# Kernel tuning notes

Hardware: AMD Instinct MI355X
Metric: run time of the kernel (lower is better)

The kernel has to match this reference:

```python
import jax, jax.numpy as jnp
import numpy as np

D_MODEL = 1024
N_HEADS = 16
D_HEAD = D_MODEL // N_HEADS
B, T = 4, 2048


def layernorm(x, g, b, eps=1e-5):
    mu = jnp.mean(x, axis=-1, keepdims=True)
    var = jnp.mean((x - mu) ** 2, axis=-1, keepdims=True)
    return (x - mu) * jax.lax.rsqrt(var + eps) * g + b


def setup_inputs() -> dict:
    key = jax.random.key(0)
    ks = jax.random.split(key, 12)
    s_in = 1.0 / np.sqrt(D_MODEL)
    s_ff = 1.0 / np.sqrt(4 * D_MODEL)
    return {
        "x": jax.random.normal(ks[0], (B, T, D_MODEL), jnp.float32),
        "Wq": jax.random.normal(ks[1], (N_HEADS, D_MODEL, D_HEAD), jnp.float32) * s_in,
        "Wk": jax.random.normal(ks[2], (N_HEADS, D_MODEL, D_HEAD), jnp.float32) * s_in,
        "Wv": jax.random.normal(ks[3], (N_HEADS, D_MODEL, D_HEAD), jnp.float32) * s_in,
        "Wproj": jax.random.normal(ks[4], (D_MODEL, D_MODEL), jnp.float32) * s_in,
        "bproj": jnp.zeros((D_MODEL,), jnp.float32),
        "W1": jax.random.normal(ks[5], (D_MODEL, 4 * D_MODEL), jnp.float32) * s_in,
        "b1": jnp.zeros((4 * D_MODEL,), jnp.float32),
        "W2": jax.random.normal(ks[6], (4 * D_MODEL, D_MODEL), jnp.float32) * s_ff,
        "b2": jnp.zeros((D_MODEL,), jnp.float32),
        "g1": jnp.ones((D_MODEL,), jnp.float32),
        "beta1": jnp.zeros((D_MODEL,), jnp.float32),
        "g2": jnp.ones((D_MODEL,), jnp.float32),
        "beta2": jnp.zeros((D_MODEL,), jnp.float32),
    }


def reference(x, Wq, Wk, Wv, Wproj, bproj, W1, b1, W2, b2, g1, beta1, g2, beta2):
    Bb, Tt, C = x.shape
    # x = ln1(x); residual uses the NORMALIZED x (quirk of original module)
    x1 = layernorm(x, g1, beta1)
    # all heads at once: [B,H,T,Dh]
    q = jnp.einsum("btd,hdk->bhtk", x1, Wq)
    k = jnp.einsum("btd,hdk->bhtk", x1, Wk)
    v = jnp.einsum("btd,hdk->bhtk", x1, Wv)
    # NOTE: original scales by 1/sqrt(C) with C = d_model, not d_head
    wei = jnp.einsum("bhtk,bhsk->bhts", q, k) / np.sqrt(C).astype(np.float32)
    causal = jnp.tril(jnp.ones((Tt, Tt), bool))
    wei = jnp.where(causal, wei, -jnp.inf)
    wei = jax.nn.softmax(wei, axis=-1)
    attn = jnp.einsum("bhts,bhsk->bhtk", wei, v)  # [B,H,T,Dh]
    attn = attn.transpose(0, 2, 1, 3).reshape(Bb, Tt, C)  # concat heads
    sa = attn @ Wproj + bproj
    x2 = x1 + sa
    # x = ln2(x); residual again uses the normalized tensor
    x3 = layernorm(x2, g2, beta2)
    h = jax.nn.relu(x3 @ W1 + b1)
    ff = h @ W2 + b2
    return x3 + ff
```

## Files before the change

kernel.cpp:

```cpp
#include <hip/hip_runtime.h>
#include <cstdint>

typedef _Float16 f16;
typedef __attribute__((ext_vector_type(8))) _Float16 f16x8;
typedef __attribute__((ext_vector_type(4))) _Float16 f16x4;
typedef __attribute__((ext_vector_type(2))) _Float16 f16x2;
typedef __attribute__((ext_vector_type(4))) float f32x4;
typedef __attribute__((ext_vector_type(16))) float f32x16;

#define D_MODEL 1024
#define T_SEQ   2048
#define NTOK    8192
#define DFF     4096
#define DHEAD   64

struct alignas(16) H8 { f16 h[8]; };

__device__ __forceinline__ void load_lds16(const void* gp, void* lp) {
  __builtin_amdgcn_global_load_lds(
      (const __attribute__((address_space(1))) unsigned int*)(unsigned long long)(uintptr_t)gp,
      (__attribute__((address_space(3))) unsigned int*)(unsigned int)(uintptr_t)lp,
      16, 0, 0);
}

__device__ __forceinline__ void phase_bar() {
  asm volatile("" ::: "memory");
  __builtin_amdgcn_sched_barrier(0);
  __builtin_amdgcn_s_barrier();
  __builtin_amdgcn_sched_barrier(0);
  asm volatile("" ::: "memory");
}

__device__ __forceinline__ void wait_vm2() {
  asm volatile("s_waitcnt vmcnt(2)" ::: "memory");
  __builtin_amdgcn_sched_barrier(0);
}
__device__ __forceinline__ void wait_vm0() {
  asm volatile("s_waitcnt vmcnt(0)" ::: "memory");
  __builtin_amdgcn_sched_barrier(0);
}

__global__ __launch_bounds__(256) void transpose_pack(
    const float* __restrict__ in, f16* __restrict__ out,
    int rows, int cols, long long in_slice, long long out_slice)
{
  __shared__ float tile[32][33];
  const float* inp = in + (size_t)blockIdx.z * in_slice;
  f16* outp = out + (size_t)blockIdx.z * out_slice;
  int r0 = blockIdx.x * 32, c0 = blockIdx.y * 32;
  int tx = threadIdx.x & 31, ty = threadIdx.x >> 5;
  #pragma unroll
  for (int i = 0; i < 4; ++i)
    tile[ty + i*8][tx] = inp[(size_t)(r0 + ty + i*8)*cols + c0 + tx];
  __syncthreads();
  #pragma unroll
  for (int i = 0; i < 4; ++i)
    outp[(size_t)(c0 + ty + i*8)*rows + r0 + tx] = (f16)tile[tx][ty + i*8];
}

__global__ __launch_bounds__(256) void ln_kernel(
    const float* __restrict__ x, const float* __restrict__ g, const float* __restrict__ b,
    float* __restrict__ outf, f16* __restrict__ outh)
{
  int row = blockIdx.x;
  const float* xr = x + (size_t)row * D_MODEL;
  int tid = threadIdx.x;
  float v[4];
  float s = 0.f;
  #pragma unroll
  for (int i = 0; i < 4; ++i) { v[i] = xr[tid + i*256]; s += v[i]; }
  #pragma unroll
  for (int off = 32; off > 0; off >>= 1) s += __shfl_down(s, off, 64);
  __shared__ float red1[4], red2[4];
  if ((tid & 63) == 0) red1[tid >> 6] = s;
  __syncthreads();
  float mean = (red1[0] + red1[1] + red1[2] + red1[3]) * (1.f / D_MODEL);
  float s2 = 0.f;
  #pragma unroll
  for (int i = 0; i < 4; ++i) { float d = v[i] - mean; s2 += d * d; }
  #pragma unroll
  for (int off = 32; off > 0; off >>= 1) s2 += __shfl_down(s2, off, 64);
  if ((tid & 63) == 0) red2[tid >> 6] = s2;
  __syncthreads();
  float var = (red2[0] + red2[1] + red2[2] + red2[3]) * (1.f / D_MODEL);
  float rstd = rsqrtf(var + 1e-5f);
  #pragma unroll
  for (int i = 0; i < 4; ++i) {
    int c = tid + i*256;
    float y = (v[i] - mean) * rstd * g[c] + b[c];
    outf[(size_t)row*D_MODEL + c] = y;
    outh[(size_t)row*D_MODEL + c] = (f16)y;
  }
}


#define STAGE_H(gbase, h, ldst, k0)                                            \
  { _Pragma("unroll")                                                          \
    for (int j_ = 0; j_ < 2; ++j_) {                                           \
      int c_  = tid + j_*512;                                                  \
      int rr_ = c_ >> 3;                                                       \
      int cg_ = (c_ & 7) ^ (rr_ & 7);                                          \
      load_lds16((gbase) + (size_t)((h)*128 + rr_) * K + (k0) + cg_*8,         \
                 (ldst) + (h)*128*64 + (size_t)(c_ & ~63) * 8);                \
    } }

#define LDS_A(bsel, mp)                                                        \
  { _Pragma("unroll")                                                          \
    for (int i_ = 0; i_ < 2; ++i_)                                             \
      _Pragma("unroll")                                                        \
      for (int ks_ = 0; ks_ < 4; ++ks_)                                        \
        fa[i_][ks_] = *(const f16x8*)(&As[bsel][                               \
            (wm + ((mp)*2 + i_)*32 + rl)*64 + (((ks_*2 + hl) ^ sw)*8)]); }

#define LDS_B(bsel, ni, fb)                                                    \
  { _Pragma("unroll")                                                          \
    for (int ks_ = 0; ks_ < 4; ++ks_)                                          \
      fb[ks_] = *(const f16x8*)(&Bs[bsel][                                     \
          (wn + (ni)*32 + rl)*64 + (((ks_*2 + hl) ^ sw)*8)]); }

#define MFMA8(mp, ni, fb)                                                      \
  { __builtin_amdgcn_s_setprio(1);                                             \
    _Pragma("unroll")                                                          \
    for (int ks_ = 0; ks_ < 4; ++ks_) {                                        \
      acc[(mp)*2+0][ni] = __builtin_amdgcn_mfma_f32_32x32x16_f16(              \
          fa[0][ks_], fb[ks_], acc[(mp)*2+0][ni], 0, 0, 0);                    \
      acc[(mp)*2+1][ni] = __builtin_amdgcn_mfma_f32_32x32x16_f16(              \
          fa[1][ks_], fb[ks_], acc[(mp)*2+1][ni], 0, 0, 0);                    \
    }                                                                          \
    __builtin_amdgcn_s_setprio(0); }

template<int MODE, int BN>
__global__ __launch_bounds__(512, 2) void gemm8(
    const f16* __restrict__ A, const f16* __restrict__ BT, int K,
    const float* __restrict__ bias, const float* __restrict__ resid,
    float* __restrict__ outf, f16* __restrict__ o0, f16* __restrict__ o1, f16* __restrict__ o2)
{
  constexpr int BM  = 256;
  constexpr int NWN = BN / 64;
  constexpr int MI  = (BM / (8 / NWN)) / 32;

  __shared__ __align__(16) f16 As[2][BM * 64];
  __shared__ __align__(16) f16 Bs[2][BN * 64];

  int tid  = threadIdx.x;
  int lane = tid & 63;
  int wave = tid >> 6;
  int rl = lane & 31, hl = lane >> 5;
  int sw = rl & 7;
  int wmi = wave / NWN, wni = wave % NWN;
  int wm = wmi * (MI * 32), wn = wni * 64;

  int gx  = gridDim.x;
  int nwg = gx * gridDim.y;
  int lin = blockIdx.x + gx * blockIdx.y;
  int sid = (nwg & 7) == 0 ? ((lin & 7) * (nwg >> 3) + (lin >> 3)) : lin;
  int bx  = sid % gx, by = sid / gx;

  size_t row0 = (size_t)bx * BM, col0 = (size_t)by * BN;
  const f16* a_base = A  + row0 * K;
  const f16* b_base = BT + col0 * K;
  int NT = K >> 6;

  f32x16 acc[MI][2];
  #pragma unroll
  for (int i = 0; i < MI; ++i)
    #pragma unroll
    for (int j = 0; j < 2; ++j)
      acc[i][j] = (f32x16)(0.f);

  f16x8 fa[2][4], fb0[4], fb1[4];

  if constexpr (BN == 256) {
    STAGE_H(a_base, 0, &As[0][0], 0);
    STAGE_H(a_base, 1, &As[0][0], 0);
    STAGE_H(b_base, 0, &Bs[0][0], 0);
    STAGE_H(b_base, 1, &Bs[0][0], 0);
    if (NT > 1) { STAGE_H(a_base, 0, &As[1][0], 64); wait_vm2(); }
    else        { wait_vm0(); }
    phase_bar();

    for (int t = 0; t < NT; ++t) {
      int cur = t & 1, nxt = cur ^ 1;
      int k1 = (t + 1) << 6, k2 = (t + 2) << 6;
      bool s1 = (t + 1) < NT, s2 = (t + 2) < NT;
      LDS_A(cur, 0); LDS_B(cur, 0, fb0);
      if (s1) STAGE_H(a_base, 1, &As[nxt][0], k1);
      phase_bar();
      MFMA8(0, 0, fb0);
      phase_bar();
      LDS_B(cur, 1, fb1);
      if (s1) STAGE_H(b_base, 0, &Bs[nxt][0], k1);
      phase_bar();
      MFMA8(0, 1, fb1);
      phase_bar();
      LDS_A(cur, 1);
      if (s1) STAGE_H(b_base, 1, &Bs[nxt][0], k1);
      phase_bar();
      MFMA8(1, 0, fb0);
      phase_bar();
      if (s2) STAGE_H(a_base, 0, &As[cur][0], k2);
      phase_bar();
      MFMA8(1, 1, fb1);
      if (s2) wait_vm2(); else wait_vm0();
      phase_bar();
    }
  } else {
    STAGE_H(a_base, 0, &As[0][0], 0);
    STAGE_H(a_base, 1, &As[0][0], 0);
    STAGE_H(b_base, 0, &Bs[0][0], 0);
    if (NT > 1) { STAGE_H(a_base, 0, &As[1][0], 64); wait_vm2(); }
    else        { wait_vm0(); }
    phase_bar();

    for (int t = 0; t < NT; t += 2) {
      int k1 = (t + 1) << 6, k2 = (t + 2) << 6, k3 = (t + 3) << 6;
      bool s1 = (t + 1) < NT, s2 = (t + 2) < NT, s3 = (t + 3) < NT;
      LDS_A(0, 0); LDS_B(0, 0, fb0);
      if (s1) { STAGE_H(a_base, 1, &As[1][0], k1); STAGE_H(b_base, 0, &Bs[1][0], k1); }
      phase_bar();
      MFMA8(0, 0, fb0);
      phase_bar();
      LDS_B(0, 1, fb1);
      if (s2) STAGE_H(a_base, 0, &As[0][0], k2);
      phase_bar();
      MFMA8(0, 1, fb1);
      if (s2) wait_vm2(); else wait_vm0();
      phase_bar();
      if (!s1) break;
      LDS_A(1, 0); LDS_B(1, 0, fb0);
      if (s2) { STAGE_H(a_base, 1, &As[0][0], k2); STAGE_H(b_base, 0, &Bs[0][0], k2); }
      phase_bar();
      MFMA8(0, 0, fb0);
      phase_bar();
      LDS_B(1, 1, fb1);
      if (s3) STAGE_H(a_base, 0, &As[1][0], k3);
      phase_bar();
      MFMA8(0, 1, fb1);
      if (s3) wait_vm2(); else wait_vm0();
      phase_bar();
    }
  }

  int rb = hl * 4;
  #pragma unroll
  for (int mi = 0; mi < MI; ++mi) {
    #pragma unroll
    for (int ni = 0; ni < 2; ++ni) {
      #pragma unroll
      for (int r = 0; r < 16; ++r) {
        size_t grow = row0 + wm + mi*32 + rb + (r & 3) + 8 * (r >> 2);
        size_t gcol = col0 + wn + ni*32 + rl;
        float v = acc[mi][ni][r];
        if constexpr (MODE == 0) {
          int sel = (int)(gcol >> 10);
          int hh  = ((int)gcol >> 6) & 15;
          int dd  = (int)gcol & 63;
          f16* dst = (sel == 0) ? o0 : ((sel == 1) ? o1 : o2);
          if (sel == 0) v *= 0.045084229f;
          size_t bh = (grow >> 11) * 16 + hh;
          dst[(bh * T_SEQ + (grow & 2047)) * DHEAD + dd] = (f16)v;
        } else if constexpr (MODE == 1 || MODE == 3) {
          size_t idx = grow * D_MODEL + gcol;
          outf[idx] = v + bias[gcol] + resid[idx];
        } else {
          float t = v + bias[gcol];
          o0[grow * (size_t)DFF + gcol] = (f16)(t > 0.f ? t : 0.f);
        }
      }
    }
  }
}

__global__ __launch_bounds__(256) void attn_mfma(
    const f16* __restrict__ qb, const f16* __restrict__ kb,
    const f16* __restrict__ vb, f16* __restrict__ attnb)
{
  constexpr int KT  = 64;
  constexpr int LDK = 72;
  __shared__ __align__(16) f16 Kl[KT * LDK];
  __shared__ __align__(16) f16 Vt[DHEAD * LDK];
  __shared__ __align__(16) f16 Pt[4 * 32 * LDK];

  int tid  = threadIdx.x;
  int lane = tid & 63, wave = tid >> 6;
  int n    = lane & 15, quad = lane >> 4;
  int quad4 = quad * 4;
  int bh   = blockIdx.y;

  const f16* qg = qb + (size_t)bh * T_SEQ * DHEAD;
  const f16* kg = kb + (size_t)bh * T_SEQ * DHEAD;
  const f16* vg = vb + (size_t)bh * T_SEQ * DHEAD;
  f16* Ptw = Pt + wave * 32 * LDK;
  size_t orow = (size_t)(bh >> 4) * T_SEQ;
  int hcol = (bh & 15) * DHEAD;

  #pragma unroll
  for (int pass = 0; pass < 2; ++pass) {
    int qi = pass == 0 ? (15 - (int)blockIdx.x) : (int)blockIdx.x;
    int qw = qi * 128 + wave * 32;

    f16x8 qfrag[2][2];
    #pragma unroll
    for (int ni = 0; ni < 2; ++ni)
      #pragma unroll
      for (int kj = 0; kj < 2; ++kj)
        qfrag[ni][kj] = *(const f16x8*)(qg + (size_t)(qw + ni*16 + n)*DHEAD + kj*32 + quad*8);

    f32x4 o[2][4];
    #pragma unroll
    for (int mb = 0; mb < 2; ++mb)
      #pragma unroll
      for (int di = 0; di < 4; ++di) o[mb][di] = f32x4{0.f,0.f,0.f,0.f};
    float lsum[2] = {0.f, 0.f};

    int ntiles = 2 * qi + 2;
    for (int kt = 0; kt < ntiles; ++kt) {
      int kt0 = kt * KT;
      __syncthreads();
      #pragma unroll
      for (int it = 0; it < 2; ++it) {
        int idx = tid + it * 256;
        int key = idx >> 3, dq = idx & 7;
        *(uint4*)(Kl + key * LDK + dq * 8) =
            *(const uint4*)(kg + (size_t)(kt0 + key) * DHEAD + dq * 8);
      }
      {
        int kp = tid & 31, dblk = tid >> 5;
        const f16* v0 = vg + (size_t)(kt0 + 2*kp) * DHEAD + dblk * 8;
        H8 va = *(const H8*)v0;
        H8 vbv = *(const H8*)(v0 + DHEAD);
        #pragma unroll
        for (int e = 0; e < 8; ++e) {
          f16x2 pk2; pk2[0] = va.h[e]; pk2[1] = vbv.h[e];
          *(f16x2*)(Vt + (dblk*8 + e) * LDK + 2*kp) = pk2;
        }
      }
      __syncthreads();

      if (kt0 > qw + 31) continue;
      bool need_mask = (kt0 + KT - 1) > qw;

      f32x4 st[4][2];
      #pragma unroll
      for (int mi = 0; mi < 4; ++mi)
        #pragma unroll
        for (int ni = 0; ni < 2; ++ni) st[mi][ni] = f32x4{0.f,0.f,0.f,0.f};
      #pragma unroll
      for (int kj = 0; kj < 2; ++kj) {
        #pragma unroll
        for (int mi = 0; mi < 4; ++mi) {
          f16x8 kf = *(const f16x8*)(Kl + (mi*16 + n) * LDK + kj*32 + quad*8);
          #pragma unroll
          for (int ni = 0; ni < 2; ++ni)
            st[mi][ni] = __builtin_amdgcn_mfma_f32_16x16x32_f16(kf, qfrag[ni][kj], st[mi][ni], 0, 0, 0);
        }
      }

      #pragma unroll
      for (int ni = 0; ni < 2; ++ni) {
        #pragma unroll
        for (int mi = 0; mi < 4; ++mi) {
          f16x4 pk;
          #pragma unroll
          for (int r = 0; r < 4; ++r) {
            float sv = st[mi][ni][r];
            if (need_mask) {
              int key = kt0 + mi*16 + quad4 + r;
              int qq  = qw  + ni*16 + n;
              if (key > qq) sv = -1e30f;
            }
            float p = __builtin_amdgcn_exp2f(sv);
            lsum[ni] += p;
            pk[r] = (f16)p;
          }
          *(f16x4*)(Ptw + (ni*16 + n) * LDK + mi*16 + quad4) = pk;
        }
      }

      #pragma unroll
      for (int kj = 0; kj < 2; ++kj) {
        f16x8 pf[2];
        #pragma unroll
        for (int mb = 0; mb < 2; ++mb)
          pf[mb] = *(const f16x8*)(Ptw + (mb*16 + n) * LDK + kj*32 + quad*8);
        #pragma unroll
        for (int di = 0; di < 4; ++di) {
          f16x8 vf = *(const f16x8*)(Vt + (di*16 + n) * LDK + kj*32 + quad*8);
          #pragma unroll
          for (int mb = 0; mb < 2; ++mb)
            o[mb][di] = __builtin_amdgcn_mfma_f32_16x16x32_f16(pf[mb], vf, o[mb][di], 0, 0, 0);
        }
      }
    }

    #pragma unroll
    for (int ni = 0; ni < 2; ++ni) {
      lsum[ni] += __shfl_xor(lsum[ni], 16, 64);
      lsum[ni] += __shfl_xor(lsum[ni], 32, 64);
    }
    #pragma unroll
    for (int mb = 0; mb < 2; ++mb) {
      #pragma unroll
      for (int r = 0; r < 4; ++r) {
        float lv  = __shfl(lsum[mb], quad4 + r, 64);
        float inv = 1.f / lv;
        int t = qw + mb*16 + quad4 + r;
        #pragma unroll
        for (int di = 0; di < 4; ++di)
          attnb[(orow + t) * D_MODEL + hcol + di*16 + n] = (f16)(o[mb][di][r] * inv);
      }
    }
  }
}

extern "C" void kernel_launch(void* const* d_in, const int* in_sizes, int n_in,
                              void* d_out, int out_size, void* d_ws, size_t ws_size,
                              hipStream_t stream)
{
  const float* x     = (const float*)d_in[0];
  const float* Wq    = (const float*)d_in[1];
  const float* Wk    = (const float*)d_in[2];
  const float* Wv    = (const float*)d_in[3];
  const float* Wproj = (const float*)d_in[4];
  const float* bproj = (const float*)d_in[5];
  const float* W1    = (const float*)d_in[6];
  const float* b1    = (const float*)d_in[7];
  const float* W2    = (const float*)d_in[8];
  const float* b2    = (const float*)d_in[9];
  const float* g1    = (const float*)d_in[10];
  const float* bt1   = (const float*)d_in[11];
  const float* g2    = (const float*)d_in[12];
  const float* bt2   = (const float*)d_in[13];
  float* out = (float*)d_out;
  (void)in_sizes; (void)n_in; (void)out_size; (void)ws_size;

  char* ws = (char*)d_ws;
  const size_t SZ_H16 = (size_t)NTOK * D_MODEL * 2;
  const size_t SZ_F32 = (size_t)NTOK * D_MODEL * 4;
  f16*   qb      = (f16*)(ws + 0);
  f16*   kb      = (f16*)(ws + 1 * SZ_H16);
  f16*   vb      = (f16*)(ws + 2 * SZ_H16);
  f16*   attnb   = (f16*)(ws + 3 * SZ_H16);
  f16*   hbuf    = (f16*)(ws + 0);
  float* x1f     = (float*)(ws + 4 * SZ_H16);
  f16*   x1h     = (f16*)(ws + 4 * SZ_H16 + SZ_F32);
  float* x3f     = (float*)(ws + 5 * SZ_H16 + SZ_F32);
  f16*   x3h     = (f16*)(ws + 5 * SZ_H16 + 2 * SZ_F32);
  char*  wb      = ws + 6 * SZ_H16 + 2 * SZ_F32;
  f16*   Wqkv_t  = (f16*)(wb);
  f16*   Wproj_t = (f16*)(wb + (size_t)3072*1024*2);
  f16*   W1_t    = (f16*)(wb + (size_t)(3072+1024)*1024*2);
  f16*   W2_t    = (f16*)(wb + (size_t)(3072+1024+4096)*1024*2);

  dim3 blk(256), blk5(512);
  transpose_pack<<<dim3(32, 2, 16), blk, 0, stream>>>(Wq, Wqkv_t,                 1024, 64,  65536, 65536);
  transpose_pack<<<dim3(32, 2, 16), blk, 0, stream>>>(Wk, Wqkv_t + 1024*1024,     1024, 64,  65536, 65536);
  transpose_pack<<<dim3(32, 2, 16), blk, 0, stream>>>(Wv, Wqkv_t + 2*1024*1024,   1024, 64,  65536, 65536);
  transpose_pack<<<dim3(32, 32, 1), blk, 0, stream>>>(Wproj, Wproj_t, 1024, 1024, 0, 0);
  transpose_pack<<<dim3(32, 128, 1), blk, 0, stream>>>(W1, W1_t, 1024, 4096, 0, 0);
  transpose_pack<<<dim3(128, 32, 1), blk, 0, stream>>>(W2, W2_t, 4096, 1024, 0, 0);
  ln_kernel<<<NTOK, blk, 0, stream>>>(x, g1, bt1, x1f, x1h);
  gemm8<0,128><<<dim3(32, 24), blk5, 0, stream>>>(x1h, Wqkv_t, 1024, nullptr, nullptr, nullptr, qb, kb, vb);
  attn_mfma<<<dim3(8, 64), blk, 0, stream>>>(qb, kb, vb, attnb);
  gemm8<1,128><<<dim3(32, 8), blk5, 0, stream>>>(attnb, Wproj_t, 1024, bproj, x1f, x1f, nullptr, nullptr, nullptr);
  ln_kernel<<<NTOK, blk, 0, stream>>>(x1f, g2, bt2, x3f, x3h);
  gemm8<2,256><<<dim3(32, 16), blk5, 0, stream>>>(x3h, W1_t, 1024, b1, nullptr, nullptr, hbuf, nullptr, nullptr);
  gemm8<3,128><<<dim3(32, 8), blk5, 0, stream>>>(hbuf, W2_t, 4096, b2, x3f, out, nullptr, nullptr, nullptr);
}
```

Measured before the change: 519.1 us.

## Split attention into one q-tile per block and prefetch next K/V tile

The attention kernel no longer processes two paired query tiles per block; instead the grid doubles to 16x64 blocks, each handling one query tile, with heaviest tiles scheduled first. K/V tiles for the next iteration are loaded into registers before the current tile's compute, hiding global-load latency behind MFMA work, and launch bounds request 4 blocks per CU. This trades the balanced-pair load scheme for more parallelism and software prefetch, at the cost of extra registers and potentially imbalanced block runtimes.

```diff
diff --git a/kernel.cpp b/kernel.cpp
--- a/kernel.cpp
+++ b/kernel.cpp
@@ -271,7 +271,7 @@
   }
 }
 
-__global__ __launch_bounds__(256) void attn_mfma(
+__global__ __launch_bounds__(256, 4) void attn_mfma(
     const f16* __restrict__ qb, const f16* __restrict__ kb,
     const f16* __restrict__ vb, f16* __restrict__ attnb)
 {
@@ -294,121 +294,129 @@
   size_t orow = (size_t)(bh >> 4) * T_SEQ;
   int hcol = (bh & 15) * DHEAD;
 
-  #pragma unroll
-  for (int pass = 0; pass < 2; ++pass) {
-    int qi = pass == 0 ? (15 - (int)blockIdx.x) : (int)blockIdx.x;
-    int qw = qi * 128 + wave * 32;
-
-    f16x8 qfrag[2][2];
-    #pragma unroll
-    for (int ni = 0; ni < 2; ++ni)
-      #pragma unroll
-      for (int kj = 0; kj < 2; ++kj)
-        qfrag[ni][kj] = *(const f16x8*)(qg + (size_t)(qw + ni*16 + n)*DHEAD + kj*32 + quad*8);
-
-    f32x4 o[2][4];
-    #pragma unroll
-    for (int mb = 0; mb < 2; ++mb)
-      #pragma unroll
-      for (int di = 0; di < 4; ++di) o[mb][di] = f32x4{0.f,0.f,0.f,0.f};
-    float lsum[2] = {0.f, 0.f};
-
-    int ntiles = 2 * qi + 2;
-    for (int kt = 0; kt < ntiles; ++kt) {
-      int kt0 = kt * KT;
-      __syncthreads();
-      #pragma unroll
-      for (int it = 0; it < 2; ++it) {
-        int idx = tid + it * 256;
-        int key = idx >> 3, dq = idx & 7;
-        *(uint4*)(Kl + key * LDK + dq * 8) =
-            *(const uint4*)(kg + (size_t)(kt0 + key) * DHEAD + dq * 8);
+  int qi = 15 - (int)blockIdx.x;
+  int qw = qi * 128 + wave * 32;
+
+  int skey0 = tid >> 3,  sdq = tid & 7;
+  int kp = tid & 31, dblk = tid >> 5;
+
+  f16x8 qfrag[2][2];
+  #pragma unroll
+  for (int ni = 0; ni < 2; ++ni)
+    #pragma unroll
+    for (int kj = 0; kj < 2; ++kj)
+      qfrag[ni][kj] = *(const f16x8*)(qg + (size_t)(qw + ni*16 + n)*DHEAD + kj*32 + quad*8);
+
+  f32x4 o[2][4];
+  #pragma unroll
+  for (int mb = 0; mb < 2; ++mb)
+    #pragma unroll
+    for (int di = 0; di < 4; ++di) o[mb][di] = f32x4{0.f,0.f,0.f,0.f};
+  float lsum[2] = {0.f, 0.f};
+
+  int ntiles = 2 * qi + 2;
+
+  uint4 kpre0, kpre1;
+  H8 vpa, vpb;
+  {
+    kpre0 = *(const uint4*)(kg + (size_t)skey0 * DHEAD + sdq * 8);
+    kpre1 = *(const uint4*)(kg + (size_t)(skey0 + 32) * DHEAD + sdq * 8);
+    const f16* v0 = vg + (size_t)(2*kp) * DHEAD + dblk * 8;
+    vpa = *(const H8*)v0;
+    vpb = *(const H8*)(v0 + DHEAD);
+  }
+
+  for (int kt = 0; kt < ntiles; ++kt) {
+    int kt0 = kt * KT;
+    __syncthreads();
+    *(uint4*)(Kl + skey0 * LDK + sdq * 8) = kpre0;
+    *(uint4*)(Kl + (skey0 + 32) * LDK + sdq * 8) = kpre1;
+    #pragma unroll
+    for (int e = 0; e < 8; ++e) {
+      f16x2 pk2; pk2[0] = vpa.h[e]; pk2[1] = vpb.h[e];
+      *(f16x2*)(Vt + (dblk*8 + e) * LDK + 2*kp) = pk2;
+    }
+    if (kt + 1 < ntiles) {
+      int nt0 = kt0 + KT;
+      kpre0 = *(const uint4*)(kg + (size_t)(nt0 + skey0) * DHEAD + sdq * 8);
+      kpre1 = *(const uint4*)(kg + (size_t)(nt0 + skey0 + 32) * DHEAD + sdq * 8);
+      const f16* v0 = vg + (size_t)(nt0 + 2*kp) * DHEAD + dblk * 8;
+      vpa = *(const H8*)v0;
+      vpb = *(const H8*)(v0 + DHEAD);
+    }
+    __syncthreads();
+
+    if (kt0 > qw + 31) continue;
+    bool need_mask = (kt0 + KT - 1) > qw;
+
+    f32x4 st[4][2];
+    #pragma unroll
+    for (int mi = 0; mi < 4; ++mi)
+      #pragma unroll
+      for (int ni = 0; ni < 2; ++ni) st[mi][ni] = f32x4{0.f,0.f,0.f,0.f};
+    #pragma unroll
+    for (int kj = 0; kj < 2; ++kj) {
+      #pragma unroll
+      for (int mi = 0; mi < 4; ++mi) {
+        f16x8 kf = *(const f16x8*)(Kl + (mi*16 + n) * LDK + kj*32 + quad*8);
+        #pragma unroll
+        for (int ni = 0; ni < 2; ++ni)
+          st[mi][ni] = __builtin_amdgcn_mfma_f32_16x16x32_f16(kf, qfrag[ni][kj], st[mi][ni], 0, 0, 0);
       }
-      {
-        int kp = tid & 31, dblk = tid >> 5;
-        const f16* v0 = vg + (size_t)(kt0 + 2*kp) * DHEAD + dblk * 8;
-        H8 va = *(const H8*)v0;
-        H8 vbv = *(const H8*)(v0 + DHEAD);
+    }
+
+    #pragma unroll
+    for (int ni = 0; ni < 2; ++ni) {
+      #pragma unroll
+      for (int mi = 0; mi < 4; ++mi) {
+        f16x4 pk;
         #pragma unroll
-        for (int e = 0; e < 8; ++e) {
-          f16x2 pk2; pk2[0] = va.h[e]; pk2[1] = vbv.h[e];
-          *(f16x2*)(Vt + (dblk*8 + e) * LDK + 2*kp) = pk2;
+        for (int r = 0; r < 4; ++r) {
+          float sv = st[mi][ni][r];
+          if (need_mask) {
+            int key = kt0 + mi*16 + quad4 + r;
+            int qq  = qw  + ni*16 + n;
+            if (key > qq) sv = -1e30f;
+          }
+          float p = __builtin_amdgcn_exp2f(sv);
+          lsum[ni] += p;
+          pk[r] = (f16)p;
         }
+        *(f16x4*)(Ptw + (ni*16 + n) * LDK + mi*16 + quad4) = pk;
       }
-      __syncthreads();
-
-      if (kt0 > qw + 31) continue;
-      bool need_mask = (kt0 + KT - 1) > qw;
-
-      f32x4 st[4][2];
-      #pragma unroll
-      for (int mi = 0; mi < 4; ++mi)
-        #pragma unroll
-        for (int ni = 0; ni < 2; ++ni) st[mi][ni] = f32x4{0.f,0.f,0.f,0.f};
-      #pragma unroll
-      for (int kj = 0; kj < 2; ++kj) {
-        #pragma unroll
-        for (int mi = 0; mi < 4; ++mi) {
-          f16x8 kf = *(const f16x8*)(Kl + (mi*16 + n) * LDK + kj*32 + quad*8);
-          #pragma unroll
-          for (int ni = 0; ni < 2; ++ni)
-            st[mi][ni] = __builtin_amdgcn_mfma_f32_16x16x32_f16(kf, qfrag[ni][kj], st[mi][ni], 0, 0, 0);
-        }
-      }
-
-      #pragma unroll
-      for (int ni = 0; ni < 2; ++ni) {
-        #pragma unroll
-        for (int mi = 0; mi < 4; ++mi) {
-          f16x4 pk;
-          #pragma unroll
-          for (int r = 0; r < 4; ++r) {
-            float sv = st[mi][ni][r];
-            if (need_mask) {
-              int key = kt0 + mi*16 + quad4 + r;
-              int qq  = qw  + ni*16 + n;
-              if (key > qq) sv = -1e30f;
-            }
-            float p = __builtin_amdgcn_exp2f(sv);
-            lsum[ni] += p;
-            pk[r] = (f16)p;
-          }
-          *(f16x4*)(Ptw + (ni*16 + n) * LDK + mi*16 + quad4) = pk;
-        }
-      }
-
-      #pragma unroll
-      for (int kj = 0; kj < 2; ++kj) {
-        f16x8 pf[2];
+    }
+
+    #pragma unroll
+    for (int kj = 0; kj < 2; ++kj) {
+      f16x8 pf[2];
+      #pragma unroll
+      for (int mb = 0; mb < 2; ++mb)
+        pf[mb] = *(const f16x8*)(Ptw + (mb*16 + n) * LDK + kj*32 + quad*8);
+      #pragma unroll
+      for (int di = 0; di < 4; ++di) {
+        f16x8 vf = *(const f16x8*)(Vt + (di*16 + n) * LDK + kj*32 + quad*8);
         #pragma unroll
         for (int mb = 0; mb < 2; ++mb)
-          pf[mb] = *(const f16x8*)(Ptw + (mb*16 + n) * LDK + kj*32 + quad*8);
-        #pragma unroll
-        for (int di = 0; di < 4; ++di) {
-          f16x8 vf = *(const f16x8*)(Vt + (di*16 + n) * LDK + kj*32 + quad*8);
-          #pragma unroll
-          for (int mb = 0; mb < 2; ++mb)
-            o[mb][di] = __builtin_amdgcn_mfma_f32_16x16x32_f16(pf[mb], vf, o[mb][di], 0, 0, 0);
-        }
+          o[mb][di] = __builtin_amdgcn_mfma_f32_16x16x32_f16(pf[mb], vf, o[mb][di], 0, 0, 0);
       }
     }
-
-    #pragma unroll
-    for (int ni = 0; ni < 2; ++ni) {
-      lsum[ni] += __shfl_xor(lsum[ni], 16, 64);
-      lsum[ni] += __shfl_xor(lsum[ni], 32, 64);
-    }
-    #pragma unroll
-    for (int mb = 0; mb < 2; ++mb) {
-      #pragma unroll
-      for (int r = 0; r < 4; ++r) {
-        float lv  = __shfl(lsum[mb], quad4 + r, 64);
-        float inv = 1.f / lv;
-        int t = qw + mb*16 + quad4 + r;
-        #pragma unroll
-        for (int di = 0; di < 4; ++di)
-          attnb[(orow + t) * D_MODEL + hcol + di*16 + n] = (f16)(o[mb][di][r] * inv);
-      }
+  }
+
+  #pragma unroll
+  for (int ni = 0; ni < 2; ++ni) {
+    lsum[ni] += __shfl_xor(lsum[ni], 16, 64);
+    lsum[ni] += __shfl_xor(lsum[ni], 32, 64);
+  }
+  #pragma unroll
+  for (int mb = 0; mb < 2; ++mb) {
+    #pragma unroll
+    for (int r = 0; r < 4; ++r) {
+      float lv  = __shfl(lsum[mb], quad4 + r, 64);
+      float inv = 1.f / lv;
+      int t = qw + mb*16 + quad4 + r;
+      #pragma unroll
+      for (int di = 0; di < 4; ++di)
+        attnb[(orow + t) * D_MODEL + hcol + di*16 + n] = (f16)(o[mb][di][r] * inv);
     }
   }
 }
@@ -461,7 +469,7 @@
   transpose_pack<<<dim3(128, 32, 1), blk, 0, stream>>>(W2, W2_t, 4096, 1024, 0, 0);
   ln_kernel<<<NTOK, blk, 0, stream>>>(x, g1, bt1, x1f, x1h);
   gemm8<0,128><<<dim3(32, 24), blk5, 0, stream>>>(x1h, Wqkv_t, 1024, nullptr, nullptr, nullptr, qb, kb, vb);
-  attn_mfma<<<dim3(8, 64), blk, 0, stream>>>(qb, kb, vb, attnb);
+  attn_mfma<<<dim3(16, 64), blk, 0, stream>>>(qb, kb, vb, attnb);
   gemm8<1,128><<<dim3(32, 8), blk5, 0, stream>>>(attnb, Wproj_t, 1024, bproj, x1f, x1f, nullptr, nullptr, nullptr);
   ln_kernel<<<NTOK, blk, 0, stream>>>(x1f, g2, bt2, x3f, x3h);
   gemm8<2,256><<<dim3(32, 16), blk5, 0, stream>>>(x3h, W1_t, 1024, b1, nullptr, nullptr, hbuf, nullptr, nullptr);
```

After: 570.8 us. +10.0%, slower.

## Double-buffer K/V tiles in attention with register prefetch; merge weight transposes

Applied to the files above, without the earlier changes.

The attention kernel now keeps two LDS buffers for K and V and prefetches the next tile's global data into registers while the current tile is being computed. This leaves one barrier per iteration instead of two and hides global load latency behind the MFMA work. The MFMA sections are also wrapped in s_setprio to raise wave priority. Separately, the six weight transpose launches are merged into one kernel that dispatches on block index, which removes launch overhead. The cost is more LDS and more registers, which may lower occupancy.

```diff
diff --git a/kernel.cpp b/kernel.cpp
--- a/kernel.cpp
+++ b/kernel.cpp
@@ -40,22 +40,46 @@
   __builtin_amdgcn_sched_barrier(0);
 }
 
-__global__ __launch_bounds__(256) void transpose_pack(
-    const float* __restrict__ in, f16* __restrict__ out,
-    int rows, int cols, long long in_slice, long long out_slice)
+__global__ __launch_bounds__(256) void transpose_all(
+    const float* __restrict__ Wq, const float* __restrict__ Wk,
+    const float* __restrict__ Wv, const float* __restrict__ Wproj,
+    const float* __restrict__ W1, const float* __restrict__ W2,
+    f16* __restrict__ Wqkv_t, f16* __restrict__ Wproj_t,
+    f16* __restrict__ W1_t, f16* __restrict__ W2_t)
 {
   __shared__ float tile[32][33];
-  const float* inp = in + (size_t)blockIdx.z * in_slice;
-  f16* outp = out + (size_t)blockIdx.z * out_slice;
-  int r0 = blockIdx.x * 32, c0 = blockIdx.y * 32;
+  int b = blockIdx.x;
+  const float* in; f16* out; int rows, cols, r0, c0;
+  if (b < 3072) {
+    int j = b >> 10;
+    int local = b & 1023;
+    int slice = local >> 6;
+    int tl = local & 63;
+    in  = (j == 0 ? Wq : (j == 1 ? Wk : Wv)) + (size_t)slice * 65536;
+    out = Wqkv_t + (size_t)j * 1024 * 1024 + (size_t)slice * 65536;
+    rows = 1024; cols = 64;
+    r0 = (tl & 31) * 32; c0 = (tl >> 5) * 32;
+  } else if (b < 4096) {
+    int tl = b - 3072;
+    in = Wproj; out = Wproj_t; rows = 1024; cols = 1024;
+    r0 = (tl & 31) * 32; c0 = (tl >> 5) * 32;
+  } else if (b < 8192) {
+    int tl = b - 4096;
+    in = W1; out = W1_t; rows = 1024; cols = 4096;
+    r0 = (tl & 31) * 32; c0 = (tl >> 5) * 32;
+  } else {
+    int tl = b - 8192;
+    in = W2; out = W2_t; rows = 4096; cols = 1024;
+    r0 = (tl & 127) * 32; c0 = (tl >> 7) * 32;
+  }
   int tx = threadIdx.x & 31, ty = threadIdx.x >> 5;
   #pragma unroll
   for (int i = 0; i < 4; ++i)
-    tile[ty + i*8][tx] = inp[(size_t)(r0 + ty + i*8)*cols + c0 + tx];
+    tile[ty + i*8][tx] = in[(size_t)(r0 + ty + i*8)*cols + c0 + tx];
   __syncthreads();
   #pragma unroll
   for (int i = 0; i < 4; ++i)
-    outp[(size_t)(c0 + ty + i*8)*rows + r0 + tx] = (f16)tile[tx][ty + i*8];
+    out[(size_t)(c0 + ty + i*8)*rows + r0 + tx] = (f16)tile[tx][ty + i*8];
 }
 
 __global__ __launch_bounds__(256) void ln_kernel(
@@ -277,8 +301,8 @@
 {
   constexpr int KT  = 64;
   constexpr int LDK = 72;
-  __shared__ __align__(16) f16 Kl[KT * LDK];
-  __shared__ __align__(16) f16 Vt[DHEAD * LDK];
+  __shared__ __align__(16) f16 Kl[2][KT * LDK];
+  __shared__ __align__(16) f16 Vt[2][DHEAD * LDK];
   __shared__ __align__(16) f16 Pt[4 * 32 * LDK];
 
   int tid  = threadIdx.x;
@@ -294,6 +318,9 @@
   size_t orow = (size_t)(bh >> 4) * T_SEQ;
   int hcol = (bh & 15) * DHEAD;
 
+  int skey0 = tid >> 3,  sdq = tid & 7;
+  int kp = tid & 31, dblk = tid >> 5;
+
   #pragma unroll
   for (int pass = 0; pass < 2; ++pass) {
     int qi = pass == 0 ? (15 - (int)blockIdx.x) : (int)blockIdx.x;
@@ -314,83 +341,109 @@
     float lsum[2] = {0.f, 0.f};
 
     int ntiles = 2 * qi + 2;
+
+    uint4 kpre0 = *(const uint4*)(kg + (size_t)skey0 * DHEAD + sdq * 8);
+    uint4 kpre1 = *(const uint4*)(kg + (size_t)(skey0 + 32) * DHEAD + sdq * 8);
+    H8 vpa = *(const H8*)(vg + (size_t)(2*kp) * DHEAD + dblk * 8);
+    H8 vpb = *(const H8*)(vg + (size_t)(2*kp) * DHEAD + DHEAD + dblk * 8);
+    *(uint4*)(&Kl[0][0] + skey0 * LDK + sdq * 8) = kpre0;
+    *(uint4*)(&Kl[0][0] + (skey0 + 32) * LDK + sdq * 8) = kpre1;
+    #pragma unroll
+    for (int e = 0; e < 8; ++e) {
+      f16x2 pk2; pk2[0] = vpa.h[e]; pk2[1] = vpb.h[e];
+      *(f16x2*)(&Vt[0][0] + (dblk*8 + e) * LDK + 2*kp) = pk2;
+    }
+    if (ntiles > 1) {
+      kpre0 = *(const uint4*)(kg + (size_t)(KT + skey0) * DHEAD + sdq * 8);
+      kpre1 = *(const uint4*)(kg + (size_t)(KT + skey0 + 32) * DHEAD + sdq * 8);
+      vpa = *(const H8*)(vg + (size_t)(KT + 2*kp) * DHEAD + dblk * 8);
+      vpb = *(const H8*)(vg + (size_t)(KT + 2*kp) * DHEAD + DHEAD + dblk * 8);
+    }
+    __syncthreads();
+
     for (int kt = 0; kt < ntiles; ++kt) {
       int kt0 = kt * KT;
-      __syncthreads();
-      #pragma unroll
-      for (int it = 0; it < 2; ++it) {
-        int idx = tid + it * 256;
-        int key = idx >> 3, dq = idx & 7;
-        *(uint4*)(Kl + key * LDK + dq * 8) =
-            *(const uint4*)(kg + (size_t)(kt0 + key) * DHEAD + dq * 8);
-      }
-      {
-        int kp = tid & 31, dblk = tid >> 5;
-        const f16* v0 = vg + (size_t)(kt0 + 2*kp) * DHEAD + dblk * 8;
-        H8 va = *(const H8*)v0;
-        H8 vbv = *(const H8*)(v0 + DHEAD);
+      if (kt + 1 < ntiles) {
+        f16* Kn = &Kl[(kt + 1) & 1][0];
+        f16* Vn = &Vt[(kt + 1) & 1][0];
+        *(uint4*)(Kn + skey0 * LDK + sdq * 8) = kpre0;
+        *(uint4*)(Kn + (skey0 + 32) * LDK + sdq * 8) = kpre1;
         #pragma unroll
         for (int e = 0; e < 8; ++e) {
-          f16x2 pk2; pk2[0] = va.h[e]; pk2[1] = vbv.h[e];
-          *(f16x2*)(Vt + (dblk*8 + e) * LDK + 2*kp) = pk2;
+          f16x2 pk2; pk2[0] = vpa.h[e]; pk2[1] = vpb.h[e];
+          *(f16x2*)(Vn + (dblk*8 + e) * LDK + 2*kp) = pk2;
+        }
+        if (kt + 2 < ntiles) {
+          int nt0 = kt0 + 2 * KT;
+          kpre0 = *(const uint4*)(kg + (size_t)(nt0 + skey0) * DHEAD + sdq * 8);
+          kpre1 = *(const uint4*)(kg + (size_t)(nt0 + skey0 + 32) * DHEAD + sdq * 8);
+          vpa = *(const H8*)(vg + (size_t)(nt0 + 2*kp) * DHEAD + dblk * 8);
+          vpb = *(const H8*)(vg + (size_t)(nt0 + 2*kp) * DHEAD + DHEAD + dblk * 8);
         }
       }
-      __syncthreads();
-
-      if (kt0 > qw + 31) continue;
-      bool need_mask = (kt0 + KT - 1) > qw;
-
-      f32x4 st[4][2];
-      #pragma unroll
-      for (int mi = 0; mi < 4; ++mi)
+
+      if (kt0 <= qw + 31) {
+        const f16* Kc = &Kl[kt & 1][0];
+        const f16* Vc = &Vt[kt & 1][0];
+        bool need_mask = (kt0 + KT - 1) > qw;
+
+        f32x4 st[4][2];
         #pragma unroll
-        for (int ni = 0; ni < 2; ++ni) st[mi][ni] = f32x4{0.f,0.f,0.f,0.f};
-      #pragma unroll
-      for (int kj = 0; kj < 2; ++kj) {
+        for (int mi = 0; mi < 4; ++mi)
+          #pragma unroll
+          for (int ni = 0; ni < 2; ++ni) st[mi][ni] = f32x4{0.f,0.f,0.f,0.f};
+        __builtin_amdgcn_s_setprio(1);
         #pragma unroll
-        for (int mi = 0; mi < 4; ++mi) {
-          f16x8 kf = *(const f16x8*)(Kl + (mi*16 + n) * LDK + kj*32 + quad*8);
+        for (int kj = 0; kj < 2; ++kj) {
           #pragma unroll
-          for (int ni = 0; ni < 2; ++ni)
-            st[mi][ni] = __builtin_amdgcn_mfma_f32_16x16x32_f16(kf, qfrag[ni][kj], st[mi][ni], 0, 0, 0);
+          for (int mi = 0; mi < 4; ++mi) {
+            f16x8 kf = *(const f16x8*)(Kc + (mi*16 + n) * LDK + kj*32 + quad*8);
+            #pragma unroll
+            for (int ni = 0; ni < 2; ++ni)
+              st[mi][ni] = __builtin_amdgcn_mfma_f32_16x16x32_f16(kf, qfrag[ni][kj], st[mi][ni], 0, 0, 0);
+          }
         }
-      }
-
-      #pragma unroll
-      for (int ni = 0; ni < 2; ++ni) {
+        __builtin_amdgcn_s_setprio(0);
+
         #pragma unroll
-        for (int mi = 0; mi < 4; ++mi) {
-          f16x4 pk;
+        for (int ni = 0; ni < 2; ++ni) {
           #pragma unroll
-          for (int r = 0; r < 4; ++r) {
-            float sv = st[mi][ni][r];
-            if (need_mask) {
-              int key = kt0 + mi*16 + quad4 + r;
-              int qq  = qw  + ni*16 + n;
-              if (key > qq) sv = -1e30f;
+          for (int mi = 0; mi < 4; ++mi) {
+            f16x4 pk;
+            #pragma unroll
+            for (int r = 0; r < 4; ++r) {
+              float sv = st[mi][ni][r];
+              if (need_mask) {
+                int key = kt0 + mi*16 + quad4 + r;
+                int qq  = qw  + ni*16 + n;
+                if (key > qq) sv = -1e30f;
+              }
+              float p = __builtin_amdgcn_exp2f(sv);
+              lsum[ni] += p;
+              pk[r] = (f16)p;
             }
-            float p = __builtin_amdgcn_exp2f(sv);
-            lsum[ni] += p;
-            pk[r] = (f16)p;
+            *(f16x4*)(Ptw + (ni*16 + n) * LDK + mi*16 + quad4) = pk;
           }
-          *(f16x4*)(Ptw + (ni*16 + n) * LDK + mi*16 + quad4) = pk;
         }
-      }
-
-      #pragma unroll
-      for (int kj = 0; kj < 2; ++kj) {
-        f16x8 pf[2];
+
+        __builtin_amdgcn_s_setprio(1);
         #pragma unroll
-        for (int mb = 0; mb < 2; ++mb)
-          pf[mb] = *(const f16x8*)(Ptw + (mb*16 + n) * LDK + kj*32 + quad*8);
-        #pragma unroll
-        for (int di = 0; di < 4; ++di) {
-          f16x8 vf = *(const f16x8*)(Vt + (di*16 + n) * LDK + kj*32 + quad*8);
+        for (int kj = 0; kj < 2; ++kj) {
+          f16x8 pf[2];
           #pragma unroll
           for (int mb = 0; mb < 2; ++mb)
-            o[mb][di] = __builtin_amdgcn_mfma_f32_16x16x32_f16(pf[mb], vf, o[mb][di], 0, 0, 0);
+            pf[mb] = *(const f16x8*)(Ptw + (mb*16 + n) * LDK + kj*32 + quad*8);
+          #pragma unroll
+          for (int di = 0; di < 4; ++di) {
+            f16x8 vf = *(const f16x8*)(Vc + (di*16 + n) * LDK + kj*32 + quad*8);
+            #pragma unroll
+            for (int mb = 0; mb < 2; ++mb)
+              o[mb][di] = __builtin_amdgcn_mfma_f32_16x16x32_f16(pf[mb], vf, o[mb][di], 0, 0, 0);
+          }
         }
+        __builtin_amdgcn_s_setprio(0);
       }
+      __syncthreads();
     }
 
     #pragma unroll
@@ -453,12 +506,8 @@
   f16*   W2_t    = (f16*)(wb + (size_t)(3072+1024+4096)*1024*2);
 
   dim3 blk(256), blk5(512);
-  transpose_pack<<<dim3(32, 2, 16), blk, 0, stream>>>(Wq, Wqkv_t,                 1024, 64,  65536, 65536);
-  transpose_pack<<<dim3(32, 2, 16), blk, 0, stream>>>(Wk, Wqkv_t + 1024*1024,     1024, 64,  65536, 65536);
-  transpose_pack<<<dim3(32, 2, 16), blk, 0, stream>>>(Wv, Wqkv_t + 2*1024*1024,   1024, 64,  65536, 65536);
-  transpose_pack<<<dim3(32, 32, 1), blk, 0, stream>>>(Wproj, Wproj_t, 1024, 1024, 0, 0);
-  transpose_pack<<<dim3(32, 128, 1), blk, 0, stream>>>(W1, W1_t, 1024, 4096, 0, 0);
-  transpose_pack<<<dim3(128, 32, 1), blk, 0, stream>>>(W2, W2_t, 4096, 1024, 0, 0);
+  transpose_all<<<dim3(12288), blk, 0, stream>>>(Wq, Wk, Wv, Wproj, W1, W2,
+                                                 Wqkv_t, Wproj_t, W1_t, W2_t);
   ln_kernel<<<NTOK, blk, 0, stream>>>(x, g1, bt1, x1f, x1h);
   gemm8<0,128><<<dim3(32, 24), blk5, 0, stream>>>(x1h, Wqkv_t, 1024, nullptr, nullptr, nullptr, qb, kb, vb);
   attn_mfma<<<dim3(8, 64), blk, 0, stream>>>(qb, kb, vb, attnb);
```

Result: no change. 514.9 us (-0.8%).
